# Kernel tuning notes

Hardware: AMD Instinct MI355X
Metric: run time of the kernel (lower is better)

Reference implementation:

```python
import jax, jax.numpy as jnp
import numpy as np

N_NODES = 8192
N_UND = 65536      # undirected pairs placed
N_DIR = 131072     # extra directed edges placed


def _build_graph():
    rng = np.random.default_rng(0)
    A = np.zeros((N_NODES, N_NODES), np.float32)
    # undirected pairs (i<j), both directions set
    ii = rng.integers(0, N_NODES, 4 * N_UND)
    jj = rng.integers(0, N_NODES, 4 * N_UND)
    m = ii < jj
    iu, ju = ii[m][:N_UND], jj[m][:N_UND]
    A[iu, ju] = 1.0
    A[ju, iu] = 1.0
    # extra directed edges
    di = rng.integers(0, N_NODES, 2 * N_DIR)
    dj = rng.integers(0, N_NODES, 2 * N_DIR)
    m2 = di != dj
    A[di[m2][:N_DIR], dj[m2][:N_DIR]] = 1.0
    # dense_to_sparse: row, col of nonzeros
    row, col = np.nonzero(A)
    edge_index = np.stack([row, col]).astype(np.int32)
    # undirected mask: A==1 & A.T==1, upper triangle
    und = np.triu((A == 1.0) & (A.T == 1.0))
    u, v = np.nonzero(und)
    undirected_edges = np.stack([u, v], axis=1).astype(np.int32)
    return A, edge_index, undirected_edges


def setup_inputs() -> dict:
    key = jax.random.key(0)
    ks = jax.random.split(key, 4)
    A, edge_index, undirected_edges = _build_graph()
    N = N_NODES
    return {
        "adjacency": jnp.asarray(A),
        "W1": jax.random.normal(ks[0], (N, 16), jnp.float32) * 0.05,
        "b1": jnp.zeros((16,), jnp.float32),
        "W2": jax.random.normal(ks[1], (16, 8), jnp.float32) * 0.25,
        "b2": jnp.zeros((8,), jnp.float32),
        "Wfc": jax.random.normal(ks[2], (16, 1), jnp.float32) * 0.25,
        "bfc": jnp.zeros((1,), jnp.float32),
        "edge_index": jnp.asarray(edge_index),
        "undirected_edges": jnp.asarray(undirected_edges),
    }


def reference(adjacency, W1, b1, W2, b2, Wfc, bfc, edge_index, undirected_edges):
    N = adjacency.shape[0]
    src, dst = edge_index[0], edge_index[1]
    E = src.shape[0]
    # GCN normalization with self-loops (PyG gcn_norm): deg over target nodes
    deg = jax.ops.segment_sum(jnp.ones((E,), adjacency.dtype), dst,
                              num_segments=N) + 1.0
    dinv = jax.lax.rsqrt(deg)                       # deg >= 1, no inf
    norm = dinv[src] * dinv[dst]                    # [E]
    self_w = (dinv * dinv)[:, None]                 # self-loop coeff [N,1]

    def conv(h):  # h: [N, F] -> normalized scatter-add aggregation
        msg = norm[:, None] * h[src]                # [E, F]
        return jax.ops.segment_sum(msg, dst, num_segments=N) + self_w * h

    # node_features = eye(N), so eye(N) @ W1 == W1
    x = jax.nn.relu(conv(W1) + b1)                  # [N, 16]
    x = jax.nn.relu(conv(x @ W2) + b2)              # [N, 8]

    u, v = undirected_edges[:, 0], undirected_edges[:, 1]
    ef = jnp.concatenate([x[u], x[v]], axis=1)      # [U, 16]
    orient = jax.nn.sigmoid(ef @ Wfc + bfc)[:, 0]   # [U]

    out = adjacency.at[u, v].set(orient).at[v, u].set(1.0 - orient)
    return out
```

## Files before the change

kernel.cpp:

```cpp
#include <hip/hip_runtime.h>
#include <math.h>

#define F1 16
#define F2 8
#define C1 4
#define C2 4

typedef float f32x4 __attribute__((ext_vector_type(4)));

__global__ void k_prep(const int* __restrict__ src, const int* __restrict__ dst,
                       int* __restrict__ degi, float* __restrict__ val,
                       int* __restrict__ rowptr, int E, int N) {
    int id = blockIdx.x * blockDim.x + threadIdx.x;
    if (id < E) {
        atomicAdd(&degi[dst[id]], 1);
        val[id] = 1.0f;
    }
    if (id <= N) {
        int lo = 0, hi = E;
        while (lo < hi) {
            int mid = (lo + hi) >> 1;
            if (src[mid] < id) lo = mid + 1; else hi = mid;
        }
        rowptr[id] = lo;
    }
}

__global__ void k_wn1(const int* __restrict__ degi, const float* __restrict__ W1,
                      float* __restrict__ dinv, float* __restrict__ Wn1, int N) {
    int id = blockIdx.x * blockDim.x + threadIdx.x;
    if (id < N * F1) {
        int i = id >> 4;
        float di = rsqrtf((float)(degi[i] + 1));
        if ((id & (F1 - 1)) == 0) dinv[i] = di;
        Wn1[id] = di * W1[id];
    }
}

__global__ void k_conv1_edges(const int* __restrict__ src, const int* __restrict__ dst,
                              const float* __restrict__ Wn1, float* __restrict__ x1,
                              int E, int N) {
    int id = blockIdx.x * blockDim.x + threadIdx.x;
    int e = id >> 4;
    int f = id & (F1 - 1);
    if (e < E) {
        int s = src[e], d = dst[e];
        float* rep = x1 + (long)(e & (C1 - 1)) * F1 * N;
        atomicAdd(&rep[(long)d * F1 + f], Wn1[(long)s * F1 + f]);
    }
}

__global__ void k_layer1(const float* __restrict__ dinv, const float* __restrict__ b1,
                         const float* __restrict__ Wn1, const float* __restrict__ W2,
                         const float* __restrict__ x1, float* __restrict__ h2n, int N) {
    int id = blockIdx.x * blockDim.x + threadIdx.x;
    if (id < N * F2) {
        int i = id >> 3;
        int g = id & (F2 - 1);
        float di = dinv[i];
        float acc = 0.0f;
        #pragma unroll
        for (int f = 0; f < F1; ++f) {
            long off = (long)i * F1 + f;
            float sum = Wn1[off];
            #pragma unroll
            for (int c = 0; c < C1; ++c) sum += x1[(long)c * F1 * N + off];
            float v = di * sum + b1[f];
            v = v > 0.0f ? v : 0.0f;
            acc += v * W2[f * F2 + g];
        }
        h2n[(long)i * F2 + g] = di * acc;
    }
}

__global__ void k_conv2_edges(const int* __restrict__ src, const int* __restrict__ dst,
                              const float* __restrict__ h2n, float* __restrict__ x2,
                              int E, int N) {
    int id = blockIdx.x * blockDim.x + threadIdx.x;
    int e = id >> 3;
    int g = id & (F2 - 1);
    if (e < E) {
        int s = src[e], d = dst[e];
        float* rep = x2 + (long)(e & (C2 - 1)) * F2 * N;
        atomicAdd(&rep[(long)d * F2 + g], h2n[(long)s * F2 + g]);
    }
}

__global__ void k_orient2(const int2* __restrict__ ue, const float* __restrict__ x2,
                          const float* __restrict__ h2n, const float* __restrict__ dinv,
                          const float* __restrict__ b2, const float* __restrict__ Wfc,
                          const float* __restrict__ bfc, const int* __restrict__ rowptr,
                          const int* __restrict__ dst, float* __restrict__ val,
                          int U, int N) {
    int k = blockIdx.x * blockDim.x + threadIdx.x;
    if (k >= U) return;
    int2 e = ue[k];
    int u = e.x, v = e.y;
    float du = dinv[u], dv = dinv[v];
    float s = bfc[0];
    #pragma unroll
    for (int g = 0; g < F2; ++g) {
        float su = h2n[(long)u * F2 + g];
        float sv = h2n[(long)v * F2 + g];
        #pragma unroll
        for (int c = 0; c < C2; ++c) {
            su += x2[(long)c * F2 * N + (long)u * F2 + g];
            sv += x2[(long)c * F2 * N + (long)v * F2 + g];
        }
        float xu = du * su + b2[g];
        float xv = dv * sv + b2[g];
        xu = xu > 0.0f ? xu : 0.0f;
        xv = xv > 0.0f ? xv : 0.0f;
        s += xu * Wfc[g] + xv * Wfc[F2 + g];
    }
    float o = 1.0f / (1.0f + expf(-s));
    int lo = rowptr[u], hi = rowptr[u + 1];
    while (lo < hi) { int mid = (lo + hi) >> 1; if (dst[mid] < v) lo = mid + 1; else hi = mid; }
    if (lo < rowptr[u + 1] && dst[lo] == v) val[lo] = o;
    lo = rowptr[v]; hi = rowptr[v + 1];
    while (lo < hi) { int mid = (lo + hi) >> 1; if (dst[mid] < u) lo = mid + 1; else hi = mid; }
    if (lo < rowptr[v + 1] && dst[lo] == u) val[lo] = 1.0f - o;
}

__global__ void __launch_bounds__(256) k_writeout(const int* __restrict__ rowptr,
                                                  const int* __restrict__ dst,
                                                  const float* __restrict__ val,
                                                  float* __restrict__ out, int N) {
    int row = blockIdx.x;
    int t = threadIdx.x;
    int n4 = N >> 2;
    f32x4* out4 = (f32x4*)(out + (long)row * N);
    f32x4 z = {0.0f, 0.0f, 0.0f, 0.0f};
    for (int j = t; j < n4; j += 256) out4[j] = z;
    __syncthreads();
    int r0 = rowptr[row], r1 = rowptr[row + 1];
    float* orow = out + (long)row * N;
    for (int k = r0 + t; k < r1; k += 256) orow[dst[k]] = val[k];
}

extern "C" void kernel_launch(void* const* d_in, const int* in_sizes, int n_in,
                              void* d_out, int out_size, void* d_ws, size_t ws_size,
                              hipStream_t stream) {
    const float* W1  = (const float*)d_in[1];
    const float* b1  = (const float*)d_in[2];
    const float* W2  = (const float*)d_in[3];
    const float* b2  = (const float*)d_in[4];
    const float* Wfc = (const float*)d_in[5];
    const float* bfc = (const float*)d_in[6];
    const int* edge_index = (const int*)d_in[7];
    const int2* und       = (const int2*)d_in[8];

    int N = in_sizes[1] / F1;
    int E = in_sizes[7] / 2;
    int U = in_sizes[8] / 2;
    const int* src = edge_index;
    const int* dst = edge_index + E;

    int*   degi   = (int*)d_ws;
    float* x1     = (float*)(degi + N);
    float* x2     = x1 + (long)C1 * F1 * N;
    float* dinv   = x2 + (long)C2 * F2 * N;
    float* Wn1    = dinv + N;
    float* h2n    = Wn1 + (long)F1 * N;
    int*   rowptr = (int*)(h2n + (long)F2 * N);
    float* val    = (float*)(rowptr + N + 1);

    const int B = 256;
    long nz = (long)N * (1 + C1 * F1 + C2 * F2);
    (void)hipMemsetAsync(d_ws, 0, (size_t)nz * sizeof(float), stream);

    {
        int work = (E > N + 1) ? E : (N + 1);
        k_prep<<<(work + B - 1) / B, B, 0, stream>>>(src, dst, degi, val, rowptr, E, N);
    }
    k_wn1<<<(N * F1 + B - 1) / B, B, 0, stream>>>(degi, W1, dinv, Wn1, N);
    {
        long work = (long)E * F1;
        k_conv1_edges<<<(int)((work + B - 1) / B), B, 0, stream>>>(src, dst, Wn1, x1, E, N);
    }
    k_layer1<<<(N * F2 + B - 1) / B, B, 0, stream>>>(dinv, b1, Wn1, W2, x1, h2n, N);
    {
        long work = (long)E * F2;
        k_conv2_edges<<<(int)((work + B - 1) / B), B, 0, stream>>>(src, dst, h2n, x2, E, N);
    }
    k_orient2<<<(U + B - 1) / B, B, 0, stream>>>(und, x2, h2n, dinv, b2, Wfc, bfc,
                                                 rowptr, dst, val, U, N);
    k_writeout<<<N, B, 0, stream>>>(rowptr, dst, val, (float*)d_out, N);
}
```

Before: 457.8 us.

## Fuse orientation into LDS-staged row writeout and drop atomic replicas

Removes the 4-way replicated atomic accumulation buffers for both convolutions, so scatter-adds go to a single array and the memset shrinks. The per-undirected-edge orient kernel and the val array are replaced by a small per-node activation kernel. Each writeout block now builds its dense row in shared memory, detects reciprocal edges with a binary search and computes the sigmoid inline, then streams the row out with nontemporal vector stores. The costs are more atomic contention on the shared accumulators, each orientation computed twice (once per direction), and 32KB of LDS per block, which may limit occupancy.

```diff
diff --git a/kernel.cpp b/kernel.cpp
--- a/kernel.cpp
+++ b/kernel.cpp
@@ -3,19 +3,13 @@
 
 #define F1 16
 #define F2 8
-#define C1 4
-#define C2 4
 
 typedef float f32x4 __attribute__((ext_vector_type(4)));
 
 __global__ void k_prep(const int* __restrict__ src, const int* __restrict__ dst,
-                       int* __restrict__ degi, float* __restrict__ val,
-                       int* __restrict__ rowptr, int E, int N) {
+                       int* __restrict__ degi, int* __restrict__ rowptr, int E, int N) {
     int id = blockIdx.x * blockDim.x + threadIdx.x;
-    if (id < E) {
-        atomicAdd(&degi[dst[id]], 1);
-        val[id] = 1.0f;
-    }
+    if (id < E) atomicAdd(&degi[dst[id]], 1);
     if (id <= N) {
         int lo = 0, hi = E;
         while (lo < hi) {
@@ -38,15 +32,13 @@
 }
 
 __global__ void k_conv1_edges(const int* __restrict__ src, const int* __restrict__ dst,
-                              const float* __restrict__ Wn1, float* __restrict__ x1,
-                              int E, int N) {
+                              const float* __restrict__ Wn1, float* __restrict__ x1, int E) {
     int id = blockIdx.x * blockDim.x + threadIdx.x;
     int e = id >> 4;
     int f = id & (F1 - 1);
     if (e < E) {
         int s = src[e], d = dst[e];
-        float* rep = x1 + (long)(e & (C1 - 1)) * F1 * N;
-        atomicAdd(&rep[(long)d * F1 + f], Wn1[(long)s * F1 + f]);
+        atomicAdd(&x1[(long)d * F1 + f], Wn1[(long)s * F1 + f]);
     }
 }
 
@@ -62,10 +54,7 @@
         #pragma unroll
         for (int f = 0; f < F1; ++f) {
             long off = (long)i * F1 + f;
-            float sum = Wn1[off];
-            #pragma unroll
-            for (int c = 0; c < C1; ++c) sum += x1[(long)c * F1 * N + off];
-            float v = di * sum + b1[f];
+            float v = di * (x1[off] + Wn1[off]) + b1[f];
             v = v > 0.0f ? v : 0.0f;
             acc += v * W2[f * F2 + g];
         }
@@ -74,68 +63,70 @@
 }
 
 __global__ void k_conv2_edges(const int* __restrict__ src, const int* __restrict__ dst,
-                              const float* __restrict__ h2n, float* __restrict__ x2,
-                              int E, int N) {
+                              const float* __restrict__ h2n, float* __restrict__ x2, int E) {
     int id = blockIdx.x * blockDim.x + threadIdx.x;
     int e = id >> 3;
     int g = id & (F2 - 1);
     if (e < E) {
         int s = src[e], d = dst[e];
-        float* rep = x2 + (long)(e & (C2 - 1)) * F2 * N;
-        atomicAdd(&rep[(long)d * F2 + g], h2n[(long)s * F2 + g]);
+        atomicAdd(&x2[(long)d * F2 + g], h2n[(long)s * F2 + g]);
     }
 }
 
-__global__ void k_orient2(const int2* __restrict__ ue, const float* __restrict__ x2,
-                          const float* __restrict__ h2n, const float* __restrict__ dinv,
-                          const float* __restrict__ b2, const float* __restrict__ Wfc,
-                          const float* __restrict__ bfc, const int* __restrict__ rowptr,
-                          const int* __restrict__ dst, float* __restrict__ val,
-                          int U, int N) {
-    int k = blockIdx.x * blockDim.x + threadIdx.x;
-    if (k >= U) return;
-    int2 e = ue[k];
-    int u = e.x, v = e.y;
-    float du = dinv[u], dv = dinv[v];
-    float s = bfc[0];
-    #pragma unroll
-    for (int g = 0; g < F2; ++g) {
-        float su = h2n[(long)u * F2 + g];
-        float sv = h2n[(long)v * F2 + g];
-        #pragma unroll
-        for (int c = 0; c < C2; ++c) {
-            su += x2[(long)c * F2 * N + (long)u * F2 + g];
-            sv += x2[(long)c * F2 * N + (long)v * F2 + g];
-        }
-        float xu = du * su + b2[g];
-        float xv = dv * sv + b2[g];
-        xu = xu > 0.0f ? xu : 0.0f;
-        xv = xv > 0.0f ? xv : 0.0f;
-        s += xu * Wfc[g] + xv * Wfc[F2 + g];
+__global__ void k_xf(const float* __restrict__ dinv, const float* __restrict__ b2,
+                     const float* __restrict__ h2n, const float* __restrict__ x2,
+                     float* __restrict__ xf, int N) {
+    int id = blockIdx.x * blockDim.x + threadIdx.x;
+    if (id < N * F2) {
+        int i = id >> 3;
+        int g = id & (F2 - 1);
+        float x = dinv[i] * (x2[id] + h2n[id]) + b2[g];
+        xf[id] = x > 0.0f ? x : 0.0f;
     }
-    float o = 1.0f / (1.0f + expf(-s));
-    int lo = rowptr[u], hi = rowptr[u + 1];
-    while (lo < hi) { int mid = (lo + hi) >> 1; if (dst[mid] < v) lo = mid + 1; else hi = mid; }
-    if (lo < rowptr[u + 1] && dst[lo] == v) val[lo] = o;
-    lo = rowptr[v]; hi = rowptr[v + 1];
-    while (lo < hi) { int mid = (lo + hi) >> 1; if (dst[mid] < u) lo = mid + 1; else hi = mid; }
-    if (lo < rowptr[v + 1] && dst[lo] == u) val[lo] = 1.0f - o;
 }
 
 __global__ void __launch_bounds__(256) k_writeout(const int* __restrict__ rowptr,
                                                   const int* __restrict__ dst,
-                                                  const float* __restrict__ val,
+                                                  const float* __restrict__ xf,
+                                                  const float* __restrict__ Wfc,
+                                                  const float* __restrict__ bfc,
                                                   float* __restrict__ out, int N) {
-    int row = blockIdx.x;
+    extern __shared__ float row[];
+    int r = blockIdx.x;
     int t = threadIdx.x;
     int n4 = N >> 2;
-    f32x4* out4 = (f32x4*)(out + (long)row * N);
+    f32x4* row4 = (f32x4*)row;
     f32x4 z = {0.0f, 0.0f, 0.0f, 0.0f};
-    for (int j = t; j < n4; j += 256) out4[j] = z;
+    for (int j = t; j < n4; j += 256) row4[j] = z;
     __syncthreads();
-    int r0 = rowptr[row], r1 = rowptr[row + 1];
-    float* orow = out + (long)row * N;
-    for (int k = r0 + t; k < r1; k += 256) orow[dst[k]] = val[k];
+    int r0 = rowptr[r], r1 = rowptr[r + 1];
+    for (int k = r0 + t; k < r1; k += 256) {
+        int c = dst[k];
+        int lo = rowptr[c], hi = rowptr[c + 1];
+        while (lo < hi) { int mid = (lo + hi) >> 1; if (dst[mid] < r) lo = mid + 1; else hi = mid; }
+        float w = 1.0f;
+        if (lo < rowptr[c + 1] && dst[lo] == r) {
+            int u = r < c ? r : c;
+            int v = r < c ? c : r;
+            const f32x4* x4 = (const f32x4*)xf;
+            f32x4 ua = x4[(long)u * 2], ub = x4[(long)u * 2 + 1];
+            f32x4 va = x4[(long)v * 2], vb = x4[(long)v * 2 + 1];
+            const f32x4* w4 = (const f32x4*)Wfc;
+            f32x4 wu0 = w4[0], wu1 = w4[1], wv0 = w4[2], wv1 = w4[3];
+            float s = bfc[0];
+            #pragma unroll
+            for (int g = 0; g < 4; ++g)
+                s += ua[g] * wu0[g] + ub[g] * wu1[g] + va[g] * wv0[g] + vb[g] * wv1[g];
+            float o = 1.0f / (1.0f + expf(-s));
+            w = (r == u) ? o : 1.0f - o;
+        }
+        row[c] = w;
+    }
+    __syncthreads();
+    f32x4* out4 = (f32x4*)(out + (long)r * N);
+    for (int j = t; j < n4; j += 256) {
+        __builtin_nontemporal_store(row4[j], &out4[j]);
+    }
 }
 
 extern "C" void kernel_launch(void* const* d_in, const int* in_sizes, int n_in,
@@ -148,42 +139,40 @@
     const float* Wfc = (const float*)d_in[5];
     const float* bfc = (const float*)d_in[6];
     const int* edge_index = (const int*)d_in[7];
-    const int2* und       = (const int2*)d_in[8];
 
     int N = in_sizes[1] / F1;
     int E = in_sizes[7] / 2;
-    int U = in_sizes[8] / 2;
     const int* src = edge_index;
     const int* dst = edge_index + E;
 
     int*   degi   = (int*)d_ws;
     float* x1     = (float*)(degi + N);
-    float* x2     = x1 + (long)C1 * F1 * N;
-    float* dinv   = x2 + (long)C2 * F2 * N;
+    float* x2     = x1 + (long)F1 * N;
+    float* dinv   = x2 + (long)F2 * N;
     float* Wn1    = dinv + N;
     float* h2n    = Wn1 + (long)F1 * N;
-    int*   rowptr = (int*)(h2n + (long)F2 * N);
-    float* val    = (float*)(rowptr + N + 1);
+    float* xf     = h2n + (long)F2 * N;
+    int*   rowptr = (int*)(xf + (long)F2 * N);
 
     const int B = 256;
-    long nz = (long)N * (1 + C1 * F1 + C2 * F2);
-    (void)hipMemsetAsync(d_ws, 0, (size_t)nz * sizeof(float), stream);
+
+    (void)hipMemsetAsync(d_ws, 0, (size_t)N * (1 + F1 + F2) * sizeof(float), stream);
 
     {
         int work = (E > N + 1) ? E : (N + 1);
-        k_prep<<<(work + B - 1) / B, B, 0, stream>>>(src, dst, degi, val, rowptr, E, N);
+        k_prep<<<(work + B - 1) / B, B, 0, stream>>>(src, dst, degi, rowptr, E, N);
     }
     k_wn1<<<(N * F1 + B - 1) / B, B, 0, stream>>>(degi, W1, dinv, Wn1, N);
     {
         long work = (long)E * F1;
-        k_conv1_edges<<<(int)((work + B - 1) / B), B, 0, stream>>>(src, dst, Wn1, x1, E, N);
+        k_conv1_edges<<<(int)((work + B - 1) / B), B, 0, stream>>>(src, dst, Wn1, x1, E);
     }
     k_layer1<<<(N * F2 + B - 1) / B, B, 0, stream>>>(dinv, b1, Wn1, W2, x1, h2n, N);
     {
         long work = (long)E * F2;
-        k_conv2_edges<<<(int)((work + B - 1) / B), B, 0, stream>>>(src, dst, h2n, x2, E, N);
+        k_conv2_edges<<<(int)((work + B - 1) / B), B, 0, stream>>>(src, dst, h2n, x2, E);
     }
-    k_orient2<<<(U + B - 1) / B, B, 0, stream>>>(und, x2, h2n, dinv, b2, Wfc, bfc,
-                                                 rowptr, dst, val, U, N);
-    k_writeout<<<N, B, 0, stream>>>(rowptr, dst, val, (float*)d_out, N);
+    k_xf<<<(N * F2 + B - 1) / B, B, 0, stream>>>(dinv, b2, h2n, x2, xf, N);
+    k_writeout<<<N, B, (size_t)N * sizeof(float), stream>>>(rowptr, dst, xf, Wfc, bfc,
+                                                            (float*)d_out, N);
 }
```

New measurement: 445.5 us. 2.7% less time.
